# Performance work log

Hardware: AMD Instinct MI355X
Metric: run time of the kernel (lower is better)

## Reference

```python
import jax, jax.numpy as jnp
import numpy as np
import math

N, D = 4096, 1024

def setup_inputs() -> dict:
    key = jax.random.key(0)
    ks = jax.random.split(key, 12)
    x = jax.random.normal(ks[0], (N, D), dtype=jnp.float32)
    attention_mask = jax.random.randint(ks[1], (N, N), 0, 2).astype(jnp.float32)
    learnable_mask = jax.random.randint(ks[2], (N, N), 0, 2).astype(jnp.float32)
    boundary_mask = jax.random.randint(ks[3], (N, 1), 0, 2).astype(jnp.float32)
    s = 1.0 / math.sqrt(D)
    W_q = jax.random.normal(ks[4], (D, D), dtype=jnp.float32) * s
    b_q = jax.random.normal(ks[5], (D,), dtype=jnp.float32) * s
    W_k = jax.random.normal(ks[6], (D, D), dtype=jnp.float32) * s
    b_k = jax.random.normal(ks[7], (D,), dtype=jnp.float32) * s
    W_v = jax.random.normal(ks[8], (D, D), dtype=jnp.float32) * s
    b_v = jax.random.normal(ks[9], (D,), dtype=jnp.float32) * s
    connection = jax.random.normal(ks[10], (D, D), dtype=jnp.float32) * s
    bias = jnp.ones((1,), dtype=jnp.float32) * 0.01
    return {"x": x, "attention_mask": attention_mask, "learnable_mask": learnable_mask,
            "boundary_mask": boundary_mask, "W_q": W_q, "b_q": b_q, "W_k": W_k, "b_k": b_k,
            "W_v": W_v, "b_v": b_v, "connection": connection, "bias": bias}

def reference(x, attention_mask, learnable_mask, boundary_mask,
              W_q, b_q, W_k, b_k, W_v, b_v, connection, bias):
    # Linear layers (torch Linear: x @ W.T + b)
    q = x @ W_q.T + b_q            # [N, D]
    k = x @ W_k.T + b_k            # [N, D]
    v = x @ W_v.T + b_v            # [N, D]
    d_head = k.shape[-1]
    attention_logits = (q @ k.T) / jnp.sqrt(jnp.asarray(d_head, x.dtype))  # [N, N]
    connection_logits = (q @ connection) @ k.T + bias                      # [N, N]
    # straight-through hard sigmoid mask
    soft_mask = jax.nn.sigmoid(connection_logits)
    st_mask = (soft_mask > 0.5).astype(x.dtype) - jax.lax.stop_gradient(soft_mask) + soft_mask
    lm = st_mask * learnable_mask
    mask = attention_mask + lm
    mask = -10000.0 * (1.0 - mask)
    attention = jax.nn.softmax(attention_logits + mask, axis=-1)  # [N, N]
    x_residual = attention @ v                                    # [N, D]
    out = boundary_mask * x_residual + (1.0 - boundary_mask) * x
    return out
```

## Files before the change

### kernel.cpp

```cpp
#include <hip/hip_runtime.h>
#include <cstdint>


typedef __attribute__((ext_vector_type(8))) short short8;
typedef __attribute__((ext_vector_type(4))) float f32x4;
typedef __attribute__((ext_vector_type(4))) float f4v;
typedef __attribute__((ext_vector_type(4))) unsigned short u16x4;
typedef __attribute__((ext_vector_type(8))) unsigned short u16x8;

typedef unsigned short u16;
typedef unsigned char u8;

__device__ __forceinline__ u16 f2bf(float f) {
  unsigned u = __float_as_uint(f);
  u += 0x7fffu + ((u >> 16) & 1u);
  return (u16)(u >> 16);
}
__device__ __forceinline__ float bf2f(u16 h) {
  return __uint_as_float(((unsigned)h) << 16);
}

__device__ __forceinline__ void gld16(void* lds, const void* g) {
  __builtin_amdgcn_global_load_lds(
      (__attribute__((address_space(1))) void*)g,
      (__attribute__((address_space(3))) void*)lds,
      16, 0, 0);
}

__global__ __launch_bounds__(256) void prep_all(
    const float* __restrict__ x, const float* __restrict__ Wq,
    const float* __restrict__ Wk, const float* __restrict__ Wv,
    const float* __restrict__ bq, const float* __restrict__ bk,
    const float* __restrict__ bv, const float* __restrict__ C,
    const float* __restrict__ bm,
    u16* __restrict__ xs3, u16* __restrict__ W3, u16* __restrict__ Wqm,
    u16* __restrict__ WqT3, u16* __restrict__ C3,
    float* __restrict__ bp, float* __restrict__ b1,
    int* __restrict__ idx, int* __restrict__ cntp) {
  __shared__ float tb[32][33];
  __shared__ int ps[256];
  const int bid = blockIdx.x, t = threadIdx.x;

  if (bid < 4096) {
    int flat = (bid * 256 + t) * 4;
    int n = flat >> 10, i = flat & 1023;
    f4v v = *(const f4v*)(x + (size_t)flat);
    u16x4 hi, lo;
#pragma unroll
    for (int e = 0; e < 4; e++) {
      u16 h = f2bf(v[e]);
      hi[e] = h;
      lo[e] = f2bf(v[e] - bf2f(h));
    }
    size_t base = (size_t)n * 3072 + i;
    *(u16x4*)(xs3 + base) = hi;
    *(u16x4*)(xs3 + base + 1024) = lo;
    *(u16x4*)(xs3 + base + 2048) = hi;
  } else if (bid < 6144) {
    int flat = ((bid - 4096) * 256 + t) * 4;
    int o = flat >> 10, i = flat & 1023;
    const float* src = (o < 1024) ? (Wk + (size_t)o * 1024)
                                  : (Wv + (size_t)(o - 1024) * 1024);
    f4v v = *(const f4v*)(src + i);
    u16x4 hi, lo;
#pragma unroll
    for (int e = 0; e < 4; e++) {
      u16 h = f2bf(v[e]);
      hi[e] = h;
      lo[e] = f2bf(v[e] - bf2f(h));
    }
    size_t base = (size_t)o * 3072 + i;
    *(u16x4*)(W3 + base) = hi;
    *(u16x4*)(W3 + base + 1024) = hi;
    *(u16x4*)(W3 + base + 2048) = lo;
  } else if (bid < 7168) {
    int flat = ((bid - 6144) * 256 + t) * 4;
    int o = flat >> 10, i = flat & 1023;
    f4v v = *(const f4v*)(Wq + (size_t)o * 1024 + i);
    u16x4 hi, lo;
#pragma unroll
    for (int e = 0; e < 4; e++) {
      u16 h = f2bf(v[e]);
      hi[e] = h;
      lo[e] = f2bf(v[e] - bf2f(h));
    }
    size_t base = (size_t)o * 3072 + i;
    *(u16x4*)(Wqm + base) = hi;
    *(u16x4*)(Wqm + base + 1024) = hi;
    *(u16x4*)(Wqm + base + 2048) = lo;
  } else if (bid < 8192) {
    int tt = bid - 7168;
    int lx = t & 31, ly = t >> 5;
    int i0 = (tt & 31) * 32, j0 = (tt >> 5) * 32;
#pragma unroll
    for (int r = 0; r < 32; r += 8)
      tb[ly + r][lx] = Wq[(size_t)(i0 + ly + r) * 1024 + j0 + lx];
    __syncthreads();
#pragma unroll
    for (int r = 0; r < 32; r += 8) {
      float f = tb[lx][ly + r];
      u16 h = f2bf(f);
      u16 l = f2bf(f - bf2f(h));
      size_t o = (size_t)(j0 + ly + r) * 3072 + i0 + lx;
      WqT3[o] = h;
      WqT3[o + 1024] = h;
      WqT3[o + 2048] = l;
    }
  } else if (bid < 9216) {
    int tt = bid - 8192;
    int lx = t & 31, ly = t >> 5;
    int i0 = (tt & 31) * 32, j0 = (tt >> 5) * 32;
#pragma unroll
    for (int r = 0; r < 32; r += 8)
      tb[ly + r][lx] = C[(size_t)(i0 + ly + r) * 1024 + j0 + lx];
    __syncthreads();
#pragma unroll
    for (int r = 0; r < 32; r += 8) {
      float f = tb[lx][ly + r];
      u16 h = f2bf(f);
      u16 l = f2bf(f - bf2f(h));
      size_t o = (size_t)(j0 + ly + r) * 3072 + i0 + lx;
      C3[o] = h;
      C3[o + 1024] = l;
      C3[o + 2048] = h;
    }
  } else if (bid < 9228) {
    int id = (bid - 9216) * 256 + t;
    float v = (id < 1024) ? bq[id] : (id < 2048) ? bk[id - 1024] : bv[id - 2048];
    bp[id] = v;
  } else if (bid == 9228) {
    int c = 0;
    for (int e = 0; e < 16; e++) {
      int r = t * 16 + e;
      if (bm[r] != 0.0f) c++;
    }
    ps[t] = c;
    __syncthreads();
    for (int off = 1; off < 256; off <<= 1) {
      int v = (t >= off) ? ps[t - off] : 0;
      __syncthreads();
      ps[t] += v;
      __syncthreads();
    }
    int p = ps[t] - c;
    for (int e = 0; e < 16; e++) {
      int r = t * 16 + e;
      if (bm[r] != 0.0f) idx[p++] = r;
    }
    int cn = ps[255];
    if (t == 0) cntp[0] = cn;
    for (int r = cn + t; r < 4096; r += 256) idx[r] = 0;
  } else {
    int j = (bid - 9229) * 256 + t;
    float a = 0.f;
    for (int d = 0; d < 1024; d++) a += bq[d] * C[(size_t)d * 1024 + j];
    b1[j] = a;
  }
}


struct EpiG1 {
  const float* bp; const float* b1;
  u16* qs; u16* k3; u16* qc3; u16* vt; int mode;
  __device__ void operator()(int r, int c, float v) const {
    if (mode == 0) {
      v += bp[1024 + c];
      u16 h = f2bf(v);
      u16 l = f2bf(v - bf2f(h));
      size_t b = (size_t)r * 3072 + c;
      k3[b] = h; k3[b + 1024] = h; k3[b + 2048] = l;
    } else if (mode == 1) {
      if (c < 1024) {
        qs[(size_t)r * 1024 + c] = f2bf(v + bp[c]);
      } else {
        float w = v + b1[c - 1024];
        u16 h = f2bf(w);
        u16 l = f2bf(w - bf2f(h));
        size_t b = (size_t)r * 3072 + (c - 1024);
        qc3[b] = h; qc3[b + 1024] = l; qc3[b + 2048] = h;
      }
    } else {
      v += bp[2048 + r];
      vt[(size_t)r * 4096 + c] = f2bf(v);
    }
  }
};

struct EpiM1 {
  float* part;
  __device__ void operator()(int r, int c, float v) const {
    part[(size_t)r * 1024 + c] = v;
  }
};

struct EpiS {
  u16* Sc;
  __device__ void operator()(int r, int c, float v) const {
    Sc[(size_t)r * 4096 + c] = f2bf(v);
  }
};

struct EpiCL {
  u8* st; float b0;
  __device__ void operator()(int r, int c, float v) const {
    st[(size_t)r * 4096 + c] = (v + b0 > 0.f) ? 1 : 0;
  }
};

struct EpiPart {
  float* part; const int* idx; int cnt;
  __device__ void operator()(int r, int c, float v) const {
    if (r < cnt) part[(size_t)idx[r] * 1024 + c] = v;
  }
};

template <class Epi>
__device__ __forceinline__ void gemm_core(
    const u16* __restrict__ A, const u16* __restrict__ B,
    int lda, int ldb, int K, int mBase, int nBase,
    const int* __restrict__ ridx, Epi epi) {
  __shared__ __align__(16) u16 lA[128 * 64];
  __shared__ __align__(16) u16 lB[128 * 64];
  const int tid = threadIdx.x;
  const int wave = tid >> 6, lane = tid & 63;
  const int wm = wave & 1, wn = wave >> 1;
  const int lane16 = lane & 15, quad = lane >> 4;

  const int srow = tid >> 3;
  const int gchunk = ((tid & 7) ^ (srow & 7)) * 8;
  const u16* aPi[4];
#pragma unroll
  for (int i = 0; i < 4; i++) {
    int row = mBase + srow + 32 * i;
    int g = ridx ? ridx[row] : row;
    aPi[i] = A + (size_t)g * lda + gchunk;
  }
  const u16* bP = B + (size_t)(nBase + srow) * ldb + gchunk;
  const int woff = wave * 1024;

  const int rsw = lane16 & 7;
  const u16* raB = lA + (wm * 64 + lane16) * 64;
  const u16* rbB = lB + (wn * 64 + lane16) * 64;

  f32x4 acc[4][4];
#pragma unroll
  for (int i = 0; i < 4; i++)
#pragma unroll
    for (int j = 0; j < 4; j++) acc[i][j] = (f32x4){0.f, 0.f, 0.f, 0.f};

  for (int k0 = 0; k0 < K; k0 += 64) {
#pragma unroll
    for (int i = 0; i < 4; i++) {
      gld16((char*)lA + i * 4096 + woff, aPi[i] + k0);
      gld16((char*)lB + i * 4096 + woff, bP + (size_t)(32 * i) * ldb + k0);
    }
    __syncthreads();
    short8 af[2][4], bfr[2][4];
#pragma unroll
    for (int s = 0; s < 2; s++) {
      const int sl = (((s << 2) + quad) ^ rsw) * 8;
#pragma unroll
      for (int j = 0; j < 4; j++) {
        af[s][j]  = *(const short8*)(raB + j * 1024 + sl);
        bfr[s][j] = *(const short8*)(rbB + j * 1024 + sl);
      }
    }
#pragma unroll
    for (int s = 0; s < 2; s++)
#pragma unroll
      for (int im = 0; im < 4; im++)
#pragma unroll
        for (int in = 0; in < 4; in++)
          acc[im][in] = __builtin_amdgcn_mfma_f32_16x16x32_bf16(
              af[s][im], bfr[s][in], acc[im][in], 0, 0, 0);
    __syncthreads();
  }

#pragma unroll
  for (int im = 0; im < 4; im++)
#pragma unroll
    for (int in = 0; in < 4; in++)
#pragma unroll
      for (int i = 0; i < 4; i++) {
        int r = mBase + wm * 64 + im * 16 + quad * 4 + i;
        int c = nBase + wn * 64 + in * 16 + lane16;
        epi(r, c, acc[im][in][i]);
      }
}

__global__ __launch_bounds__(256, 2) void gemm_m1(
    const u16* __restrict__ C3, const u16* __restrict__ WqT3,
    float* __restrict__ parts) {
  const int z = blockIdx.x >> 6, tile = blockIdx.x & 63;
  gemm_core(C3 + z * 768, WqT3 + z * 768, 3072, 3072, 768,
            (tile >> 3) * 128, (tile & 7) * 128, nullptr,
            EpiM1{parts + (size_t)z * 1024 * 1024});
}

__global__ void m1fin(const float* __restrict__ parts, u16* __restrict__ Wqm) {
  int flat = (blockIdx.x * 256 + threadIdx.x) * 4;
  int j = flat >> 10, i = flat & 1023;
  const size_t SL = (size_t)1024 * 1024;
  f4v p0 = *(const f4v*)(parts + (size_t)flat);
  f4v p1 = *(const f4v*)(parts + SL + flat);
  f4v p2 = *(const f4v*)(parts + 2 * SL + flat);
  f4v p3 = *(const f4v*)(parts + 3 * SL + flat);
  u16x4 hi, lo;
#pragma unroll
  for (int e = 0; e < 4; e++) {
    float f = (p0[e] + p1[e]) + (p2[e] + p3[e]);
    u16 h = f2bf(f);
    hi[e] = h;
    lo[e] = f2bf(f - bf2f(h));
  }
  size_t base = (size_t)(1024 + j) * 3072 + i;
  *(u16x4*)(Wqm + base) = hi;
  *(u16x4*)(Wqm + base + 1024) = hi;
  *(u16x4*)(Wqm + base + 2048) = lo;
}

__global__ __launch_bounds__(256, 2) void gemm_g1(
    const u16* __restrict__ xs3, const u16* __restrict__ W3,
    const u16* __restrict__ Wqm, const float* __restrict__ bp,
    const float* __restrict__ b1, u16* __restrict__ qs,
    u16* __restrict__ k3, u16* __restrict__ qc3, u16* __restrict__ vt,
    const int* __restrict__ idx, const int* __restrict__ cntp) {
  const int bid = blockIdx.x;
  const int sel = bid & 3;
  const u16 *A, *B;
  const int* rx = nullptr;
  int K, mB, nB, mode;
  if (sel < 3) {
    const int L = (bid >> 2) * 3 + sel;
    if (L < 256) {
      A = xs3; B = W3; K = 3072;
      mB = (L >> 3) * 128; nB = (L & 7) * 128; mode = 0;
    } else {
      const int t = L - 256;
      mB = (t >> 4) * 128;
      if (mB >= cntp[0]) return;
      A = xs3; B = Wqm; K = 3072; nB = (t & 15) * 128; rx = idx; mode = 1;
    }
  } else {
    const int s = bid >> 2;
    A = W3 + (size_t)1024 * 3072; B = xs3; K = 1024;
    mB = (s & 7) * 128; nB = (s >> 3) * 128; mode = 2;
  }
  gemm_core(A, B, 3072, 3072, K, mB, nB, rx,
            EpiG1{bp, b1, qs, k3, qc3, vt, mode});
}

__global__ __launch_bounds__(256, 2) void gemm_s(
    const u16* __restrict__ qs, const u16* __restrict__ k3,
    u16* __restrict__ Sc, const int* __restrict__ cntp) {
  const int t = blockIdx.x;
  const int mB = (t >> 5) * 128;
  if (mB >= cntp[0]) return;
  gemm_core(qs, k3, 1024, 3072, 1024, mB, (t & 31) * 128, nullptr, EpiS{Sc});
}

__global__ __launch_bounds__(256, 2) void gemm_cl(
    const u16* __restrict__ qc3, const u16* __restrict__ k3,
    const float* __restrict__ bias, u8* __restrict__ st,
    const int* __restrict__ cntp) {
  const int bid = blockIdx.x;
  const int mBase = (bid >> 5) * 128;
  if (mBase >= cntp[0]) return;
  gemm_core(qc3, k3, 3072, 3072, 3072, mBase, (bid & 31) * 128, nullptr,
            EpiCL{st, bias[0]});
}

__global__ __launch_bounds__(256, 2) void gemm_pv(
    const u16* __restrict__ P, const u16* __restrict__ vt,
    float* __restrict__ p01, float* __restrict__ p23,
    const int* __restrict__ idx, const int* __restrict__ cntp) {
  const int bid = blockIdx.x;
  const int z = bid >> 8, rem = bid & 255;
  const int cnt = cntp[0];
  const int mBase = (rem >> 3) * 128;
  if (mBase >= cnt) return;
  float* base = ((z < 2) ? p01 : p23) + (size_t)(z & 1) * (4096ull * 1024ull);
  const size_t kOff = (size_t)z * 1024;
  gemm_core(P + kOff, vt + kOff, 4096, 4096, 1024, mBase, (rem & 7) * 128,
            nullptr, EpiPart{base, idx, cnt});
}

__global__ void reduce_out(const float* __restrict__ x, const float* __restrict__ bm,
                           const float* __restrict__ p01, const float* __restrict__ p23,
                           float* __restrict__ out) {
  int id = blockIdx.x * 256 + threadIdx.x;
  int flat = id * 4;
  int r = flat >> 10;
  float b = bm[r];
  f4v xv = *(const f4v*)(x + (size_t)flat);
  f4v o;
  if (b != 0.0f) {
    const size_t SL = (size_t)4096 * 1024;
    f4v a0 = *(const f4v*)(p01 + (size_t)flat);
    f4v a1 = *(const f4v*)(p01 + SL + flat);
    f4v a2 = *(const f4v*)(p23 + (size_t)flat);
    f4v a3 = *(const f4v*)(p23 + SL + flat);
#pragma unroll
    for (int e = 0; e < 4; e++)
      o[e] = b * ((a0[e] + a1[e]) + (a2[e] + a3[e])) + (1.0f - b) * xv[e];
  } else {
    o = xv;
  }
  *(f4v*)(out + (size_t)flat) = o;
}

__global__ __launch_bounds__(256) void mask_softmax(
    const u16* __restrict__ Sc, const u8* __restrict__ st,
    const float* __restrict__ am, const float* __restrict__ lm,
    u16* __restrict__ P, const int* __restrict__ idx,
    const int* __restrict__ cntp) {
  const int n = blockIdx.x, tid = threadIdx.x;
  if (n >= cntp[0]) return;
  const int orow = idx[n];
  const int lane = tid & 63, wave = tid >> 6;
  const u16* Srow = Sc + (size_t)n * 4096;
  const u8* Trow = st + (size_t)n * 4096;
  const float* Arow = am + (size_t)orow * 4096;
  const float* Lrow = lm + (size_t)orow * 4096;

  float lg[16];
  float mx = -3.4e38f;
#pragma unroll
  for (int j = 0; j < 2; j++) {
    int base = (tid + 256 * j) * 8;
    u16x8 s8 = *(const u16x8*)(Srow + base);
    unsigned long long t8 = *(const unsigned long long*)(Trow + base);
    f4v a0 = *(const f4v*)(Arow + base), a1 = *(const f4v*)(Arow + base + 4);
    f4v l0 = *(const f4v*)(Lrow + base), l1 = *(const f4v*)(Lrow + base + 4);
#pragma unroll
    for (int e = 0; e < 8; e++) {
      float stv = ((t8 >> (8 * e)) & 1ull) ? 1.f : 0.f;
      float a = (e < 4) ? a0[e] : a1[e - 4];
      float l = (e < 4) ? l0[e] : l1[e - 4];
      float mv = a + stv * l;
      float v = bf2f(s8[e]) * 0.03125f - 10000.f * (1.f - mv);
      lg[j * 8 + e] = v;
      mx = fmaxf(mx, v);
    }
  }
#pragma unroll
  for (int o = 32; o; o >>= 1) mx = fmaxf(mx, __shfl_xor(mx, o));
  __shared__ float smax[4], ssum[4];
  if (lane == 0) smax[wave] = mx;
  __syncthreads();
  mx = fmaxf(fmaxf(smax[0], smax[1]), fmaxf(smax[2], smax[3]));

  float sum = 0.f;
#pragma unroll
  for (int i = 0; i < 16; i++) { lg[i] = __expf(lg[i] - mx); sum += lg[i]; }
#pragma unroll
  for (int o = 32; o; o >>= 1) sum += __shfl_xor(sum, o);
  if (lane == 0) ssum[wave] = sum;
  __syncthreads();
  float inv = 1.f / (ssum[0] + ssum[1] + ssum[2] + ssum[3]);

  u16* Pr = P + (size_t)n * 4096;
#pragma unroll
  for (int j = 0; j < 2; j++) {
    int base = (tid + 256 * j) * 8;
    u16x8 o8;
#pragma unroll
    for (int e = 0; e < 8; e++) o8[e] = f2bf(lg[j * 8 + e] * inv);
    *(u16x8*)(Pr + base) = o8;
  }
}


extern "C" void kernel_launch(void* const* d_in, const int* in_sizes, int n_in,
                              void* d_out, int out_size, void* d_ws, size_t ws_size,
                              hipStream_t stream) {
  const float* x    = (const float*)d_in[0];
  const float* am   = (const float*)d_in[1];
  const float* lm   = (const float*)d_in[2];
  const float* bm   = (const float*)d_in[3];
  const float* Wq   = (const float*)d_in[4];
  const float* bq   = (const float*)d_in[5];
  const float* Wk   = (const float*)d_in[6];
  const float* bk   = (const float*)d_in[7];
  const float* Wv   = (const float*)d_in[8];
  const float* bv   = (const float*)d_in[9];
  const float* Cc   = (const float*)d_in[10];
  const float* bias = (const float*)d_in[11];
  float* out = (float*)d_out;
  char* ws = (char*)d_ws;

  if (ws_size < 0xB010000) return;

  u16*  xs3  = (u16*) (ws + 0x0000000);
  u16*  W3   = (u16*) (ws + 0x1800000);
  u16*  Wqm  = (u16*) (ws + 0x2400000);
  u16*  C3   = (u16*) (ws + 0x3000000);
  u16*  WqT3 = (u16*) (ws + 0x3600000);
  float* bp  = (float*)(ws + 0x3C00000);
  float* b1  = (float*)(ws + 0x3C04000);
  int*  idx  = (int*)  (ws + 0x3C08000);
  int*  cnt  = (int*)  (ws + 0x3C0C000);
  u16*  qs   = (u16*) (ws + 0x3D00000);
  u16*  qc3  = (u16*) (ws + 0x4500000);
  u16*  k3   = (u16*) (ws + 0x5D00000);
  u16*  vt   = (u16*) (ws + 0x7500000);
  u16*  Sc   = (u16*) (ws + 0x7D00000);
  u8*   st   = (u8*)  (ws + 0x9D00000);
  float* m1parts = (float*)(ws + 0x7D00000);
  u16*  P    = (u16*) (ws + 0x0000000);
  float* parts01 = (float*)(ws + 0x4500000);
  float* parts23 = (float*)(ws + 0x7D00000);

  prep_all<<<9233, 256, 0, stream>>>(x, Wq, Wk, Wv, bq, bk, bv, Cc, bm,
                                     xs3, W3, Wqm, WqT3, C3, bp, b1, idx, cnt);
  gemm_m1<<<256, 256, 0, stream>>>(C3, WqT3, m1parts);
  m1fin<<<1024, 256, 0, stream>>>(m1parts, Wqm);
  gemm_g1<<<1024, 256, 0, stream>>>(xs3, W3, Wqm, bp, b1, qs, k3, qc3, vt,
                                    idx, cnt);
  gemm_s<<<1024, 256, 0, stream>>>(qs, k3, Sc, cnt);
  gemm_cl<<<1024, 256, 0, stream>>>(qc3, k3, bias, st, cnt);
  mask_softmax<<<4096, 256, 0, stream>>>(Sc, st, am, lm, P, idx, cnt);
  gemm_pv<<<1024, 256, 0, stream>>>(P, vt, parts01, parts23, idx, cnt);
  reduce_out<<<4096, 256, 0, stream>>>(x, bm, parts01, parts23, out);
}
```

Before: 450.6 us.

## Merge S and CL GEMMs into one launch and rebalance G1/PV block scheduling

Fuses the separate S-score and connection-logit GEMM kernels into one kernel with 2048 blocks. The expensive CL tiles come first and the cheaper S tiles after, so the two share the GPU and there is one fewer launch. Shrinks gemm_g1 to 768 blocks, where the first 256 blocks each compute two tiles (a K=3072 tile and a K=1024 V tile). Reorders gemm_pv block indexing so the K-split partials of the same row tile are adjacent, which may improve cache reuse of P. The risks are load imbalance from the serial two-tile blocks in g1 and extra branching in the shared epilogue.

```diff
diff --git a/kernel.cpp b/kernel.cpp
--- a/kernel.cpp
+++ b/kernel.cpp
@@ -193,17 +193,11 @@
   }
 };
 
-struct EpiS {
-  u16* Sc;
+struct EpiSCL {
+  u16* Sc; u8* st; float b0; int isS;
   __device__ void operator()(int r, int c, float v) const {
-    Sc[(size_t)r * 4096 + c] = f2bf(v);
-  }
-};
-
-struct EpiCL {
-  u8* st; float b0;
-  __device__ void operator()(int r, int c, float v) const {
-    st[(size_t)r * 4096 + c] = (v + b0 > 0.f) ? 1 : 0;
+    if (isS) Sc[(size_t)r * 4096 + c] = f2bf(v);
+    else st[(size_t)r * 4096 + c] = (v + b0 > 0.f) ? 1 : 0;
   }
 };
 
@@ -326,48 +320,52 @@
     u16* __restrict__ k3, u16* __restrict__ qc3, u16* __restrict__ vt,
     const int* __restrict__ idx, const int* __restrict__ cntp) {
   const int bid = blockIdx.x;
-  const int sel = bid & 3;
-  const u16 *A, *B;
-  const int* rx = nullptr;
-  int K, mB, nB, mode;
-  if (sel < 3) {
-    const int L = (bid >> 2) * 3 + sel;
-    if (L < 256) {
-      A = xs3; B = W3; K = 3072;
-      mB = (L >> 3) * 128; nB = (L & 7) * 128; mode = 0;
+  const int cnt = cntp[0];
+  for (int j = 0; j < 2; ++j) {
+    const u16 *A, *B;
+    const int* rx = nullptr;
+    int K, mB, nB, mode;
+    if (j == 0) {
+      if (bid < 256) {
+        A = xs3; B = W3; K = 3072;
+        mB = (bid >> 3) * 128; nB = (bid & 7) * 128; mode = 0;
+      } else {
+        const int t = bid - 256;
+        mB = (t >> 4) * 128;
+        if (mB >= cnt) continue;
+        A = xs3; B = Wqm; K = 3072; nB = (t & 15) * 128; rx = idx; mode = 1;
+      }
     } else {
-      const int t = L - 256;
-      mB = (t >> 4) * 128;
-      if (mB >= cntp[0]) return;
-      A = xs3; B = Wqm; K = 3072; nB = (t & 15) * 128; rx = idx; mode = 1;
-    }
-  } else {
-    const int s = bid >> 2;
-    A = W3 + (size_t)1024 * 3072; B = xs3; K = 1024;
-    mB = (s & 7) * 128; nB = (s >> 3) * 128; mode = 2;
-  }
-  gemm_core(A, B, 3072, 3072, K, mB, nB, rx,
-            EpiG1{bp, b1, qs, k3, qc3, vt, mode});
-}
-
-__global__ __launch_bounds__(256, 2) void gemm_s(
-    const u16* __restrict__ qs, const u16* __restrict__ k3,
-    u16* __restrict__ Sc, const int* __restrict__ cntp) {
-  const int t = blockIdx.x;
-  const int mB = (t >> 5) * 128;
-  if (mB >= cntp[0]) return;
-  gemm_core(qs, k3, 1024, 3072, 1024, mB, (t & 31) * 128, nullptr, EpiS{Sc});
-}
-
-__global__ __launch_bounds__(256, 2) void gemm_cl(
-    const u16* __restrict__ qc3, const u16* __restrict__ k3,
-    const float* __restrict__ bias, u8* __restrict__ st,
+      if (bid >= 256) break;
+      A = W3 + (size_t)1024 * 3072; B = xs3; K = 1024;
+      mB = (bid & 7) * 128; nB = (bid >> 3) * 128; mode = 2;
+    }
+    gemm_core(A, B, 3072, 3072, K, mB, nB, rx,
+              EpiG1{bp, b1, qs, k3, qc3, vt, mode});
+  }
+}
+
+__global__ __launch_bounds__(256, 2) void gemm_scl(
+    const u16* __restrict__ qs, const u16* __restrict__ qc3,
+    const u16* __restrict__ k3, const float* __restrict__ bias,
+    u16* __restrict__ Sc, u8* __restrict__ st,
     const int* __restrict__ cntp) {
   const int bid = blockIdx.x;
-  const int mBase = (bid >> 5) * 128;
-  if (mBase >= cntp[0]) return;
-  gemm_core(qc3, k3, 3072, 3072, 3072, mBase, (bid & 31) * 128, nullptr,
-            EpiCL{st, bias[0]});
+  const int cnt = cntp[0];
+  const u16* A;
+  int lda, K, mB, nB, isS;
+  if (bid < 1024) {
+    mB = (bid >> 5) * 128;
+    if (mB >= cnt) return;
+    A = qc3; lda = 3072; K = 3072; nB = (bid & 31) * 128; isS = 0;
+  } else {
+    const int t = bid - 1024;
+    mB = (t >> 5) * 128;
+    if (mB >= cnt) return;
+    A = qs; lda = 1024; K = 1024; nB = (t & 31) * 128; isS = 1;
+  }
+  gemm_core(A, k3, lda, 3072, K, mB, nB, nullptr,
+            EpiSCL{Sc, st, bias[0], isS});
 }
 
 __global__ __launch_bounds__(256, 2) void gemm_pv(
@@ -375,13 +373,14 @@
     float* __restrict__ p01, float* __restrict__ p23,
     const int* __restrict__ idx, const int* __restrict__ cntp) {
   const int bid = blockIdx.x;
-  const int z = bid >> 8, rem = bid & 255;
+  const int m = bid >> 5, rem = bid & 31;
+  const int z = rem >> 3, n = rem & 7;
   const int cnt = cntp[0];
-  const int mBase = (rem >> 3) * 128;
+  const int mBase = m * 128;
   if (mBase >= cnt) return;
   float* base = ((z < 2) ? p01 : p23) + (size_t)(z & 1) * (4096ull * 1024ull);
   const size_t kOff = (size_t)z * 1024;
-  gemm_core(P + kOff, vt + kOff, 4096, 4096, 1024, mBase, (rem & 7) * 128,
+  gemm_core(P + kOff, vt + kOff, 4096, 4096, 1024, mBase, n * 128,
             nullptr, EpiPart{base, idx, cnt});
 }
 
@@ -515,10 +514,9 @@
                                      xs3, W3, Wqm, WqT3, C3, bp, b1, idx, cnt);
   gemm_m1<<<256, 256, 0, stream>>>(C3, WqT3, m1parts);
   m1fin<<<1024, 256, 0, stream>>>(m1parts, Wqm);
-  gemm_g1<<<1024, 256, 0, stream>>>(xs3, W3, Wqm, bp, b1, qs, k3, qc3, vt,
-                                    idx, cnt);
-  gemm_s<<<1024, 256, 0, stream>>>(qs, k3, Sc, cnt);
-  gemm_cl<<<1024, 256, 0, stream>>>(qc3, k3, bias, st, cnt);
+  gemm_g1<<<768, 256, 0, stream>>>(xs3, W3, Wqm, bp, b1, qs, k3, qc3, vt,
+                                   idx, cnt);
+  gemm_scl<<<2048, 256, 0, stream>>>(qs, qc3, k3, bias, Sc, st, cnt);
   mask_softmax<<<4096, 256, 0, stream>>>(Sc, st, am, lm, P, idx, cnt);
   gemm_pv<<<1024, 256, 0, stream>>>(P, vt, parts01, parts23, idx, cnt);
   reduce_out<<<4096, 256, 0, stream>>>(x, bm, parts01, parts23, out);
```

Result: faster. 427.3 us (-5.2%).
